# Kernel optimization log

Measured on AMD Instinct MI355X. Metric: run time of the kernel, lower is better.

Reference implementation:

```python
import jax, jax.numpy as jnp
import numpy as np

N, E = 8000, 128000
IN_DIM = OUT_DIM = REL_DIM = 64
NUM_RELS, NUM_BASES = 200, 50
R2 = 2 * NUM_RELS


def setup_inputs() -> dict:
    key = jax.random.key(0)
    ks = jax.random.split(key, 10)
    feat = jax.random.normal(ks[0], (N, IN_DIM), jnp.float32)
    rel_emb = jax.random.normal(ks[1], (R2, REL_DIM), jnp.float32)
    weight = jax.random.normal(ks[2], (NUM_BASES, IN_DIM, OUT_DIM), jnp.float32) * 0.05
    w_comp = jax.random.normal(ks[3], (R2, NUM_BASES), jnp.float32) * 0.1
    self_loop_weight = jax.random.normal(ks[4], (IN_DIM, OUT_DIM), jnp.float32) * 0.05
    W_R_w = jax.random.normal(ks[5], (REL_DIM, REL_DIM), jnp.float32) * 0.05
    W_R_b = jnp.zeros((REL_DIM,), jnp.float32)
    src = jax.random.randint(ks[6], (E,), 0, N, dtype=jnp.int32)
    dst = jax.random.randint(ks[7], (E,), 0, N, dtype=jnp.int32)
    etype = jax.random.randint(ks[8], (E,), 0, R2, dtype=jnp.int32)
    return dict(feat=feat, rel_emb=rel_emb, weight=weight, w_comp=w_comp,
                self_loop_weight=self_loop_weight, W_R_w=W_R_w, W_R_b=W_R_b,
                src=src, dst=dst, etype=etype)


def reference(feat, rel_emb, weight, w_comp, self_loop_weight, W_R_w, W_R_b,
              src, dst, etype):
    # rel_weight = (w_comp @ weight.view(B, in*out)).view(R2, in, out)
    rel_weight = jnp.einsum('rb,bio->rio', w_comp, weight)          # [R2, in, out]
    # msg_func: per-edge relation weight gather + bmm (gather-mm pattern)
    w_e = rel_weight[etype]                                          # [E, in, out]
    msg = jnp.einsum('ei,eio->eo', feat[src], w_e)                   # [E, out]
    # aggregator: alpha = 1/in_deg(dst) per edge -> weighted sum == mean over mailbox
    ones = jnp.ones((msg.shape[0],), msg.dtype)
    in_deg = jax.ops.segment_sum(ones, dst, num_segments=N)          # [N]
    nei_sum = jax.ops.segment_sum(msg, dst, num_segments=N)          # [N, out]
    nei_msg = nei_sum / jnp.maximum(in_deg, 1.0)[:, None]
    # curr_emb = dst_feat @ self_loop_weight (same for every edge into a node)
    curr_emb = feat @ self_loop_weight                               # [N, out]
    h = curr_emb + nei_msg                                           # no bias / no activation
    # is_input_layer=True: repr = cat([feat, h])
    repr_ = jnp.concatenate([feat, h], axis=1)                       # [N, in+out]
    # edge_update: W_R linear on relation embeddings (act is None)
    rel_emb_new = rel_emb @ W_R_w.T + W_R_b                          # [R2, rel_dim]
    return repr_, rel_emb_new
```

## Files before the change

### kernel.cpp

```cpp
#include <hip/hip_runtime.h>

#define N_NODES 8000
#define E_EDGES 128000
#define NUM_BASES 50
#define R2 400
#define CPR 4
#define RT 16

static __device__ __forceinline__ float bf2f(unsigned short u) {
    return __uint_as_float(((unsigned int)u) << 16);
}
static __device__ __forceinline__ unsigned short f2bf(float f) {
    unsigned int u = __float_as_uint(f);
    u += 0x7fffu + ((u >> 16) & 1u);
    return (unsigned short)(u >> 16);
}
static __device__ __forceinline__ float bcast(float v, int lane) {
    return __uint_as_float(__builtin_amdgcn_readlane(__float_as_uint(v), lane));
}

__global__ __launch_bounds__(256) void k_zero(int4* __restrict__ p, int n4) {
    const int i = blockIdx.x * 256 + threadIdx.x;
    if (i < n4) p[i] = make_int4(0, 0, 0, 0);
}

__global__ __launch_bounds__(256) void k_pre(const float* __restrict__ w_comp,
                                             const float* __restrict__ weight,
                                             unsigned short* __restrict__ relWh,
                                             const int* __restrict__ dst,
                                             const int* __restrict__ etype,
                                             int* __restrict__ cnt16,
                                             int* __restrict__ dcnt) {
    const int blk = blockIdx.x;
    const int t = threadIdx.x;
    if (blk < 100) {
        const int rt = blk >> 2;
        const int pb = blk & 3;
        const int r0 = rt * RT;
        const int p = pb * 256 + t;
        const float4* w4 = (const float4*)weight;
        float4 acc[RT];
#pragma unroll
        for (int rr = 0; rr < RT; ++rr) acc[rr] = make_float4(0.f, 0.f, 0.f, 0.f);
        for (int b = 0; b < NUM_BASES; ++b) {
            const float4 w = w4[b * 1024 + p];
#pragma unroll
            for (int rr = 0; rr < RT; ++rr) {
                const float c = w_comp[(r0 + rr) * NUM_BASES + b];
                acc[rr].x = fmaf(c, w.x, acc[rr].x);
                acc[rr].y = fmaf(c, w.y, acc[rr].y);
                acc[rr].z = fmaf(c, w.z, acc[rr].z);
                acc[rr].w = fmaf(c, w.w, acc[rr].w);
            }
        }
        ushort4* outh = (ushort4*)relWh;
#pragma unroll
        for (int rr = 0; rr < RT; ++rr) {
            ushort4 v;
            v.x = f2bf(acc[rr].x); v.y = f2bf(acc[rr].y);
            v.z = f2bf(acc[rr].z); v.w = f2bf(acc[rr].w);
            outh[(r0 + rr) * 1024 + p] = v;
        }
    } else {
        const int e = (blk - 100) * 256 + t;
        if (e >= E_EDGES) return;
        atomicAdd(&cnt16[etype[e] * 16], 1);
        atomicAdd(&dcnt[dst[e]], 1);
    }
}

__global__ __launch_bounds__(1024) void k_scan(const int* __restrict__ cnt16,
                                               const int* __restrict__ dcnt,
                                               int* __restrict__ off,
                                               int* __restrict__ doff,
                                               int* __restrict__ cursor16,
                                               int* __restrict__ dcursor) {
    __shared__ int s[1024];
    const int t = threadIdx.x;
    if (blockIdx.x == 0) {
        const int v = (t < R2) ? cnt16[t * 16] : 0;
        s[t] = v;
        __syncthreads();
        for (int d = 1; d < 1024; d <<= 1) {
            const int p = (t >= d) ? s[t - d] : 0;
            __syncthreads();
            s[t] += p;
            __syncthreads();
        }
        if (t == 0) off[0] = 0;
        if (t < R2) {
            off[t + 1] = s[t];
            cursor16[t * 16] = s[t] - v;
        }
    } else {
        const int base = t * 8;
        int loc[8];
        int run = 0;
#pragma unroll
        for (int q = 0; q < 8; ++q) {
            const int v = (base + q < N_NODES) ? dcnt[base + q] : 0;
            loc[q] = run;
            run += v;
        }
        s[t] = run;
        __syncthreads();
        for (int d = 1; d < 1024; d <<= 1) {
            const int p = (t >= d) ? s[t - d] : 0;
            __syncthreads();
            s[t] += p;
            __syncthreads();
        }
        const int ex = s[t] - run;
#pragma unroll
        for (int q = 0; q < 8; ++q) {
            if (base + q < N_NODES) {
                const int o = ex + loc[q];
                doff[base + q] = o;
                dcursor[base + q] = o;
            }
        }
        if (t == 1023) doff[N_NODES] = s[1023];
    }
}

__global__ __launch_bounds__(256) void k_scatter(const int* __restrict__ src,
                                                 const int* __restrict__ dst,
                                                 const int* __restrict__ etype,
                                                 int* __restrict__ cursor16,
                                                 int* __restrict__ dcursor,
                                                 int2* __restrict__ sedge,
                                                 int mode) {
    const int e = blockIdx.x * 256 + threadIdx.x;
    if (e >= E_EDGES) return;
    const int r = etype[e];
    const int d = dst[e];
    const int rpos = atomicAdd(&cursor16[r * 16], 1);
    int y;
    if (mode == 0) y = atomicAdd(&dcursor[d], 1);
    else           y = d;
    sedge[rpos] = make_int2(src[e], y);
}

__global__ __launch_bounds__(256) void k_edge(const float* __restrict__ feat,
                                              const unsigned short* __restrict__ relWh,
                                              const int2* __restrict__ sedge,
                                              const int* __restrict__ off,
                                              unsigned short* __restrict__ msg) {
    const int xcd = blockIdx.x & 7;
    const int j = blockIdx.x >> 3;
    const int r = xcd * 50 + (j >> 2);
    const int chunk = j & 3;
    const int lane = threadIdx.x & 63;
    const int wv = threadIdx.x >> 6;
    const int beg = off[r];
    const int cnt = off[r + 1] - beg;
    const int cbeg = beg + (cnt * chunk) / CPR;
    const int cend = beg + (cnt * (chunk + 1)) / CPR;

    const unsigned short* __restrict__ Wh = relWh + r * 4096;
    float w[64];
#pragma unroll
    for (int i = 0; i < 64; ++i) w[i] = bf2f(Wh[i * 64 + lane]);

    int idx = cbeg + wv;
    for (; idx + 4 < cend; idx += 8) {
        const int iB = idx + 4;
        const int2 eA = sedge[idx];
        const int2 eB = sedge[iB];
        const int sA = __builtin_amdgcn_readfirstlane(eA.x);
        const int dA = __builtin_amdgcn_readfirstlane(eA.y);
        const int sB = __builtin_amdgcn_readfirstlane(eB.x);
        const int dB = __builtin_amdgcn_readfirstlane(eB.y);
        const float* __restrict__ fA = feat + sA * 64;
        const float* __restrict__ fB = feat + sB * 64;
        float a0 = 0.f, a1 = 0.f, a2 = 0.f, a3 = 0.f;
        float b0 = 0.f, b1 = 0.f, b2 = 0.f, b3 = 0.f;
#pragma unroll
        for (int i = 0; i < 64; i += 4) {
            a0 = fmaf(fA[i    ], w[i    ], a0);  b0 = fmaf(fB[i    ], w[i    ], b0);
            a1 = fmaf(fA[i + 1], w[i + 1], a1);  b1 = fmaf(fB[i + 1], w[i + 1], b1);
            a2 = fmaf(fA[i + 2], w[i + 2], a2);  b2 = fmaf(fB[i + 2], w[i + 2], b2);
            a3 = fmaf(fA[i + 3], w[i + 3], a3);  b3 = fmaf(fB[i + 3], w[i + 3], b3);
        }
        msg[dA * 64 + lane] = f2bf((a0 + a1) + (a2 + a3));
        msg[dB * 64 + lane] = f2bf((b0 + b1) + (b2 + b3));
    }
    for (; idx < cend; idx += 4) {
        const int2 eA = sedge[idx];
        const int sA = __builtin_amdgcn_readfirstlane(eA.x);
        const int dA = __builtin_amdgcn_readfirstlane(eA.y);
        const float* __restrict__ frow = feat + sA * 64;
        float a0 = 0.f, a1 = 0.f, a2 = 0.f, a3 = 0.f;
#pragma unroll
        for (int i = 0; i < 64; i += 4) {
            a0 = fmaf(frow[i    ], w[i    ], a0);
            a1 = fmaf(frow[i + 1], w[i + 1], a1);
            a2 = fmaf(frow[i + 2], w[i + 2], a2);
            a3 = fmaf(frow[i + 3], w[i + 3], a3);
        }
        msg[dA * 64 + lane] = f2bf((a0 + a1) + (a2 + a3));
    }
}

__global__ __launch_bounds__(256) void k_edge_at(const float* __restrict__ feat,
                                                 const unsigned short* __restrict__ relWh,
                                                 const int2* __restrict__ sedge,
                                                 const int* __restrict__ off,
                                                 float* __restrict__ nei_sum) {
    const int xcd = blockIdx.x & 7;
    const int j = blockIdx.x >> 3;
    const int r = xcd * 50 + (j >> 2);
    const int chunk = j & 3;
    const int lane = threadIdx.x & 63;
    const int wv = threadIdx.x >> 6;
    const int beg = off[r];
    const int cnt = off[r + 1] - beg;
    const int cbeg = beg + (cnt * chunk) / CPR;
    const int cend = beg + (cnt * (chunk + 1)) / CPR;

    const unsigned short* __restrict__ Wh = relWh + r * 4096;
    float w[64];
#pragma unroll
    for (int i = 0; i < 64; ++i) w[i] = bf2f(Wh[i * 64 + lane]);

    for (int idx = cbeg + wv; idx < cend; idx += 4) {
        const int2 eA = sedge[idx];
        const int s = __builtin_amdgcn_readfirstlane(eA.x);
        const int d = __builtin_amdgcn_readfirstlane(eA.y);
        const float* __restrict__ frow = feat + s * 64;
        float a0 = 0.f, a1 = 0.f, a2 = 0.f, a3 = 0.f;
#pragma unroll
        for (int i = 0; i < 64; i += 4) {
            a0 = fmaf(frow[i    ], w[i    ], a0);
            a1 = fmaf(frow[i + 1], w[i + 1], a1);
            a2 = fmaf(frow[i + 2], w[i + 2], a2);
            a3 = fmaf(frow[i + 3], w[i + 3], a3);
        }
        atomicAdd(&nei_sum[d * 64 + lane], (a0 + a1) + (a2 + a3));
    }
}

__global__ __launch_bounds__(256) void k_post(const float* __restrict__ feat,
                                              const float* __restrict__ slw,
                                              const int* __restrict__ doff,
                                              const unsigned short* __restrict__ msg,
                                              const float* __restrict__ rel_emb,
                                              const float* __restrict__ Wr,
                                              const float* __restrict__ br,
                                              float* __restrict__ out) {
    __shared__ float s_w[4096];
    const int blk = blockIdx.x;
    const int t = threadIdx.x;
    const int lane = t & 63;
    const int wv = t >> 6;
    if (blk < 500) {
#pragma unroll
        for (int k = 0; k < 16; ++k) s_w[k * 256 + t] = slw[k * 256 + t];
        __syncthreads();
#pragma unroll
        for (int q = 0; q < 4; ++q) {
            const int n = blk * 16 + wv * 4 + q;
            const int b0 = doff[n];
            const int b1 = doff[n + 1];
            const float* __restrict__ frow = feat + n * 64;
            const float fa = frow[lane];
            float acc = 0.f;
#pragma unroll
            for (int i = 0; i < 64; ++i)
                acc = fmaf(frow[i], s_w[i * 64 + lane], acc);
            float sm = 0.f;
            int jj = b0;
            for (; jj + 1 < b1; jj += 2) {
                const float m0 = bf2f(msg[jj * 64 + lane]);
                const float m1 = bf2f(msg[(jj + 1) * 64 + lane]);
                sm += m0 + m1;
            }
            if (jj < b1) sm += bf2f(msg[jj * 64 + lane]);
            const float inv = 1.0f / fmaxf((float)(b1 - b0), 1.0f);
            out[n * 128 + lane] = fa;
            out[n * 128 + 64 + lane] = fmaf(sm, inv, acc);
        }
    } else {
#pragma unroll
        for (int k = 0; k < 16; ++k) {
            const int idx = k * 256 + t;
            s_w[(idx & 63) * 64 + (idx >> 6)] = Wr[idx];
        }
        __syncthreads();
        const int r = (blk - 500) * 4 + wv;
        const float re = rel_emb[r * 64 + lane];
        float acc = br[lane];
#pragma unroll
        for (int k = 0; k < 64; ++k)
            acc = fmaf(bcast(re, k), s_w[k * 64 + lane], acc);
        out[N_NODES * 128 + r * 64 + lane] = acc;
    }
}

__global__ __launch_bounds__(256) void k_post_at(const float* __restrict__ feat,
                                                 const float* __restrict__ slw,
                                                 const float* __restrict__ nei_sum,
                                                 const int* __restrict__ doff,
                                                 const float* __restrict__ rel_emb,
                                                 const float* __restrict__ Wr,
                                                 const float* __restrict__ br,
                                                 float* __restrict__ out) {
    __shared__ float s_w[4096];
    const int blk = blockIdx.x;
    const int t = threadIdx.x;
    const int lane = t & 63;
    const int wv = t >> 6;
    if (blk < 500) {
#pragma unroll
        for (int k = 0; k < 16; ++k) s_w[k * 256 + t] = slw[k * 256 + t];
        __syncthreads();
#pragma unroll
        for (int q = 0; q < 4; ++q) {
            const int n = blk * 16 + wv * 4 + q;
            const float* __restrict__ frow = feat + n * 64;
            const float fa = frow[lane];
            float acc = 0.f;
#pragma unroll
            for (int i = 0; i < 64; ++i)
                acc = fmaf(frow[i], s_w[i * 64 + lane], acc);
            const float deg = (float)(doff[n + 1] - doff[n]);
            const float inv = 1.0f / fmaxf(deg, 1.0f);
            out[n * 128 + lane] = fa;
            out[n * 128 + 64 + lane] = fmaf(nei_sum[n * 64 + lane], inv, acc);
        }
    } else {
#pragma unroll
        for (int k = 0; k < 16; ++k) {
            const int idx = k * 256 + t;
            s_w[(idx & 63) * 64 + (idx >> 6)] = Wr[idx];
        }
        __syncthreads();
        const int r = (blk - 500) * 4 + wv;
        const float re = rel_emb[r * 64 + lane];
        float acc = br[lane];
#pragma unroll
        for (int k = 0; k < 64; ++k)
            acc = fmaf(bcast(re, k), s_w[k * 64 + lane], acc);
        out[N_NODES * 128 + r * 64 + lane] = acc;
    }
}

extern "C" void kernel_launch(void* const* d_in, const int* in_sizes, int n_in,
                              void* d_out, int out_size, void* d_ws, size_t ws_size,
                              hipStream_t stream) {
    const float* feat    = (const float*)d_in[0];
    const float* rel_emb = (const float*)d_in[1];
    const float* weight  = (const float*)d_in[2];
    const float* w_comp  = (const float*)d_in[3];
    const float* slw     = (const float*)d_in[4];
    const float* Wr      = (const float*)d_in[5];
    const float* br      = (const float*)d_in[6];
    const int*   src     = (const int*)d_in[7];
    const int*   dst     = (const int*)d_in[8];
    const int*   etype   = (const int*)d_in[9];
    float* out = (float*)d_out;
    char* ws = (char*)d_ws;

    if (ws_size >= 20833728) {
        unsigned short* relWh = (unsigned short*)(ws);
        unsigned short* msg   = (unsigned short*)(ws + 3276800);
        int2* sedge   = (int2*)(ws + 19660800);
        int* off      = (int*)(ws + 20684800);
        int* doff     = (int*)(ws + 20686464);
        int* cnt16    = (int*)(ws + 20718528);
        int* dcnt     = (int*)(ws + 20744128);
        int* cursor16 = (int*)(ws + 20776128);
        int* dcursor  = (int*)(ws + 20801728);

        k_zero<<<15, 256, 0, stream>>>((int4*)cnt16, 3600);
        k_pre<<<600, 256, 0, stream>>>(w_comp, weight, relWh, dst, etype,
                                       cnt16, dcnt);
        k_scan<<<2, 1024, 0, stream>>>(cnt16, dcnt, off, doff, cursor16, dcursor);
        k_scatter<<<500, 256, 0, stream>>>(src, dst, etype, cursor16, dcursor,
                                           sedge, 0);
        k_edge<<<R2 * CPR, 256, 0, stream>>>(feat, relWh, sedge, off, msg);
        k_post<<<600, 256, 0, stream>>>(feat, slw, doff, msg, rel_emb, Wr, br,
                                        out);
    } else {
        unsigned short* relWh = (unsigned short*)(ws);
        int2* sedge   = (int2*)(ws + 3276800);
        int* off      = (int*)(ws + 4300800);
        int* doff     = (int*)(ws + 4302464);
        float* nei    = (float*)(ws + 4334528);
        int* cnt16    = (int*)(ws + 6382528);
        int* dcnt     = (int*)(ws + 6408128);
        int* cursor16 = (int*)(ws + 6440128);
        int* dcursor  = (int*)(ws + 6465728);

        k_zero<<<515, 256, 0, stream>>>((int4*)nei, 131600);
        k_pre<<<600, 256, 0, stream>>>(w_comp, weight, relWh, dst, etype,
                                       cnt16, dcnt);
        k_scan<<<2, 1024, 0, stream>>>(cnt16, dcnt, off, doff, cursor16, dcursor);
        k_scatter<<<500, 256, 0, stream>>>(src, dst, etype, cursor16, dcursor,
                                           sedge, 1);
        k_edge_at<<<R2 * CPR, 256, 0, stream>>>(feat, relWh, sedge, off, nei);
        k_post_at<<<600, 256, 0, stream>>>(feat, slw, nei, doff, rel_emb, Wr, br,
                                           out);
    }
}
```

Before: 119.1 us.

## Use per-block LDS histograms for edge bucketing and single-wave edge blocks

```diff
diff --git a/kernel.cpp b/kernel.cpp
--- a/kernel.cpp
+++ b/kernel.cpp
@@ -4,8 +4,10 @@
 #define E_EDGES 128000
 #define NUM_BASES 50
 #define R2 400
-#define CPR 4
+#define CPR 8
 #define RT 16
+#define HB 32
+#define EPB (E_EDGES / HB)
 
 static __device__ __forceinline__ float bf2f(unsigned short u) {
     return __uint_as_float(((unsigned int)u) << 16);
@@ -29,8 +31,8 @@
                                              unsigned short* __restrict__ relWh,
                                              const int* __restrict__ dst,
                                              const int* __restrict__ etype,
-                                             int* __restrict__ cnt16,
-                                             int* __restrict__ dcnt) {
+                                             int* __restrict__ bcnt,
+                                             int* __restrict__ dcnt16) {
     const int blk = blockIdx.x;
     const int t = threadIdx.x;
     if (blk < 100) {
@@ -62,96 +64,125 @@
             outh[(r0 + rr) * 1024 + p] = v;
         }
     } else {
-        const int e = (blk - 100) * 256 + t;
-        if (e >= E_EDGES) return;
-        atomicAdd(&cnt16[etype[e] * 16], 1);
-        atomicAdd(&dcnt[dst[e]], 1);
-    }
-}
-
-__global__ __launch_bounds__(1024) void k_scan(const int* __restrict__ cnt16,
-                                               const int* __restrict__ dcnt,
-                                               int* __restrict__ off,
-                                               int* __restrict__ doff,
-                                               int* __restrict__ cursor16,
-                                               int* __restrict__ dcursor) {
-    __shared__ int s[1024];
+        __shared__ int lcnt[R2];
+        const int hb = blk - 100;
+        for (int i = t; i < R2; i += 256) lcnt[i] = 0;
+        __syncthreads();
+        const int e0 = hb * EPB;
+        for (int e = e0 + t; e < e0 + EPB; e += 256) {
+            atomicAdd(&lcnt[etype[e]], 1);
+            atomicAdd(&dcnt16[dst[e] * 16], 1);
+        }
+        __syncthreads();
+        for (int i = t; i < R2; i += 256) bcnt[hb * R2 + i] = lcnt[i];
+    }
+}
+
+__global__ __launch_bounds__(512) void k_scan(const int* __restrict__ bcnt,
+                                              const int* __restrict__ dcnt16,
+                                              int* __restrict__ off,
+                                              int* __restrict__ doff,
+                                              int* __restrict__ bbase,
+                                              int* __restrict__ dcursor16) {
+    __shared__ int sh[8];
     const int t = threadIdx.x;
+    const int lane = t & 63;
+    const int wid = t >> 6;
     if (blockIdx.x == 0) {
-        const int v = (t < R2) ? cnt16[t * 16] : 0;
-        s[t] = v;
-        __syncthreads();
-        for (int d = 1; d < 1024; d <<= 1) {
-            const int p = (t >= d) ? s[t - d] : 0;
-            __syncthreads();
-            s[t] += p;
-            __syncthreads();
-        }
+        int tot = 0;
+        if (t < R2)
+            for (int b = 0; b < HB; ++b) tot += bcnt[b * R2 + t];
+        int v = tot;
+#pragma unroll
+        for (int d = 1; d < 64; d <<= 1) {
+            const int u = __shfl_up(v, d, 64);
+            if (lane >= d) v += u;
+        }
+        if (lane == 63) sh[wid] = v;
+        __syncthreads();
+        int wo = 0;
+        for (int i = 0; i < wid; ++i) wo += sh[i];
+        const int incl = v + wo;
+        const int ex = incl - tot;
         if (t == 0) off[0] = 0;
         if (t < R2) {
-            off[t + 1] = s[t];
-            cursor16[t * 16] = s[t] - v;
+            off[t + 1] = incl;
+            int run = ex;
+            for (int b = 0; b < HB; ++b) {
+                bbase[b * R2 + t] = run;
+                run += bcnt[b * R2 + t];
+            }
         }
     } else {
-        const int base = t * 8;
-        int loc[8];
+        int loc[32];
         int run = 0;
-#pragma unroll
-        for (int q = 0; q < 8; ++q) {
-            const int v = (base + q < N_NODES) ? dcnt[base + q] : 0;
-            loc[q] = run;
-            run += v;
-        }
-        s[t] = run;
-        __syncthreads();
-        for (int d = 1; d < 1024; d <<= 1) {
-            const int p = (t >= d) ? s[t - d] : 0;
-            __syncthreads();
-            s[t] += p;
-            __syncthreads();
-        }
-        const int ex = s[t] - run;
-#pragma unroll
-        for (int q = 0; q < 8; ++q) {
-            if (base + q < N_NODES) {
-                const int o = ex + loc[q];
-                doff[base + q] = o;
-                dcursor[base + q] = o;
-            }
-        }
-        if (t == 1023) doff[N_NODES] = s[1023];
+        const int base = t * 32;
+        if (t < 256) {
+#pragma unroll
+            for (int q = 0; q < 32; ++q) {
+                const int v = (base + q < N_NODES) ? dcnt16[(base + q) * 16] : 0;
+                loc[q] = run;
+                run += v;
+            }
+        }
+        int v = (t < 256) ? run : 0;
+#pragma unroll
+        for (int d = 1; d < 64; d <<= 1) {
+            const int u = __shfl_up(v, d, 64);
+            if (lane >= d) v += u;
+        }
+        if (lane == 63 && wid < 4) sh[wid] = v;
+        __syncthreads();
+        if (t < 256) {
+            int wo = 0;
+            for (int i = 0; i < wid; ++i) wo += sh[i];
+            const int incl = v + wo;
+            const int ex = incl - run;
+#pragma unroll
+            for (int q = 0; q < 32; ++q) {
+                if (base + q < N_NODES) {
+                    const int o = ex + loc[q];
+                    doff[base + q] = o;
+                    dcursor16[(base + q) * 16] = o;
+                }
+            }
+            if (t == 255) doff[N_NODES] = incl;
+        }
     }
 }
 
 __global__ __launch_bounds__(256) void k_scatter(const int* __restrict__ src,
                                                  const int* __restrict__ dst,
                                                  const int* __restrict__ etype,
-                                                 int* __restrict__ cursor16,
-                                                 int* __restrict__ dcursor,
-                                                 int2* __restrict__ sedge,
-                                                 int mode) {
-    const int e = blockIdx.x * 256 + threadIdx.x;
-    if (e >= E_EDGES) return;
-    const int r = etype[e];
-    const int d = dst[e];
-    const int rpos = atomicAdd(&cursor16[r * 16], 1);
-    int y;
-    if (mode == 0) y = atomicAdd(&dcursor[d], 1);
-    else           y = d;
-    sedge[rpos] = make_int2(src[e], y);
-}
-
-__global__ __launch_bounds__(256) void k_edge(const float* __restrict__ feat,
-                                              const unsigned short* __restrict__ relWh,
-                                              const int2* __restrict__ sedge,
-                                              const int* __restrict__ off,
-                                              unsigned short* __restrict__ msg) {
-    const int xcd = blockIdx.x & 7;
-    const int j = blockIdx.x >> 3;
-    const int r = xcd * 50 + (j >> 2);
-    const int chunk = j & 3;
-    const int lane = threadIdx.x & 63;
-    const int wv = threadIdx.x >> 6;
+                                                 const int* __restrict__ bbase,
+                                                 int* __restrict__ dcursor16,
+                                                 int2* __restrict__ sedge) {
+    __shared__ int lcur[R2];
+    const int blk = blockIdx.x;
+    const int t = threadIdx.x;
+    for (int i = t; i < R2; i += 256) lcur[i] = bbase[blk * R2 + i];
+    __syncthreads();
+    const int e0 = blk * EPB;
+    for (int e = e0 + t; e < e0 + EPB; e += 256) {
+        const int r = etype[e];
+        const int d = dst[e];
+        const int rpos = atomicAdd(&lcur[r], 1);
+        const int dpos = atomicAdd(&dcursor16[d * 16], 1);
+        sedge[rpos] = make_int2(src[e], dpos);
+    }
+}
+
+__global__ __launch_bounds__(64, 1) void k_edge(const float* __restrict__ feat,
+                                                const unsigned short* __restrict__ relWh,
+                                                const int2* __restrict__ sedge,
+                                                const int* __restrict__ off,
+                                                unsigned short* __restrict__ msg) {
+    const int blk = blockIdx.x;
+    const int xcd = blk & 7;
+    const int j = blk >> 3;
+    const int r = xcd * 50 + (j >> 3);
+    const int chunk = j & 7;
+    const int lane = threadIdx.x;
     const int beg = off[r];
     const int cnt = off[r + 1] - beg;
     const int cbeg = beg + (cnt * chunk) / CPR;
@@ -162,11 +193,10 @@
 #pragma unroll
     for (int i = 0; i < 64; ++i) w[i] = bf2f(Wh[i * 64 + lane]);
 
-    int idx = cbeg + wv;
-    for (; idx + 4 < cend; idx += 8) {
-        const int iB = idx + 4;
+    int idx = cbeg;
+    for (; idx + 1 < cend; idx += 2) {
         const int2 eA = sedge[idx];
-        const int2 eB = sedge[iB];
+        const int2 eB = sedge[idx + 1];
         const int sA = __builtin_amdgcn_readfirstlane(eA.x);
         const int dA = __builtin_amdgcn_readfirstlane(eA.y);
         const int sB = __builtin_amdgcn_readfirstlane(eB.x);
@@ -185,7 +215,7 @@
         msg[dA * 64 + lane] = f2bf((a0 + a1) + (a2 + a3));
         msg[dB * 64 + lane] = f2bf((b0 + b1) + (b2 + b3));
     }
-    for (; idx < cend; idx += 4) {
+    if (idx < cend) {
         const int2 eA = sedge[idx];
         const int sA = __builtin_amdgcn_readfirstlane(eA.x);
         const int dA = __builtin_amdgcn_readfirstlane(eA.y);
@@ -199,44 +229,6 @@
             a3 = fmaf(frow[i + 3], w[i + 3], a3);
         }
         msg[dA * 64 + lane] = f2bf((a0 + a1) + (a2 + a3));
-    }
-}
-
-__global__ __launch_bounds__(256) void k_edge_at(const float* __restrict__ feat,
-                                                 const unsigned short* __restrict__ relWh,
-                                                 const int2* __restrict__ sedge,
-                                                 const int* __restrict__ off,
-                                                 float* __restrict__ nei_sum) {
-    const int xcd = blockIdx.x & 7;
-    const int j = blockIdx.x >> 3;
-    const int r = xcd * 50 + (j >> 2);
-    const int chunk = j & 3;
-    const int lane = threadIdx.x & 63;
-    const int wv = threadIdx.x >> 6;
-    const int beg = off[r];
-    const int cnt = off[r + 1] - beg;
-    const int cbeg = beg + (cnt * chunk) / CPR;
-    const int cend = beg + (cnt * (chunk + 1)) / CPR;
-
-    const unsigned short* __restrict__ Wh = relWh + r * 4096;
-    float w[64];
-#pragma unroll
-    for (int i = 0; i < 64; ++i) w[i] = bf2f(Wh[i * 64 + lane]);
-
-    for (int idx = cbeg + wv; idx < cend; idx += 4) {
-        const int2 eA = sedge[idx];
-        const int s = __builtin_amdgcn_readfirstlane(eA.x);
-        const int d = __builtin_amdgcn_readfirstlane(eA.y);
-        const float* __restrict__ frow = feat + s * 64;
-        float a0 = 0.f, a1 = 0.f, a2 = 0.f, a3 = 0.f;
-#pragma unroll
-        for (int i = 0; i < 64; i += 4) {
-            a0 = fmaf(frow[i    ], w[i    ], a0);
-            a1 = fmaf(frow[i + 1], w[i + 1], a1);
-            a2 = fmaf(frow[i + 2], w[i + 2], a2);
-            a3 = fmaf(frow[i + 3], w[i + 3], a3);
-        }
-        atomicAdd(&nei_sum[d * 64 + lane], (a0 + a1) + (a2 + a3));
     }
 }
 
@@ -270,63 +262,17 @@
                 acc = fmaf(frow[i], s_w[i * 64 + lane], acc);
             float sm = 0.f;
             int jj = b0;
-            for (; jj + 1 < b1; jj += 2) {
+            for (; jj + 3 < b1; jj += 4) {
                 const float m0 = bf2f(msg[jj * 64 + lane]);
                 const float m1 = bf2f(msg[(jj + 1) * 64 + lane]);
-                sm += m0 + m1;
-            }
-            if (jj < b1) sm += bf2f(msg[jj * 64 + lane]);
+                const float m2 = bf2f(msg[(jj + 2) * 64 + lane]);
+                const float m3 = bf2f(msg[(jj + 3) * 64 + lane]);
+                sm += (m0 + m1) + (m2 + m3);
+            }
+            for (; jj < b1; ++jj) sm += bf2f(msg[jj * 64 + lane]);
             const float inv = 1.0f / fmaxf((float)(b1 - b0), 1.0f);
             out[n * 128 + lane] = fa;
             out[n * 128 + 64 + lane] = fmaf(sm, inv, acc);
-        }
-    } else {
-#pragma unroll
-        for (int k = 0; k < 16; ++k) {
-            const int idx = k * 256 + t;
-            s_w[(idx & 63) * 64 + (idx >> 6)] = Wr[idx];
-        }
-        __syncthreads();
-        const int r = (blk - 500) * 4 + wv;
-        const float re = rel_emb[r * 64 + lane];
-        float acc = br[lane];
-#pragma unroll
-        for (int k = 0; k < 64; ++k)
-            acc = fmaf(bcast(re, k), s_w[k * 64 + lane], acc);
-        out[N_NODES * 128 + r * 64 + lane] = acc;
-    }
-}
-
-__global__ __launch_bounds__(256) void k_post_at(const float* __restrict__ feat,
-                                                 const float* __restrict__ slw,
-                                                 const float* __restrict__ nei_sum,
-                                                 const int* __restrict__ doff,
-                                                 const float* __restrict__ rel_emb,
-                                                 const float* __restrict__ Wr,
-                                                 const float* __restrict__ br,
-                                                 float* __restrict__ out) {
-    __shared__ float s_w[4096];
-    const int blk = blockIdx.x;
-    const int t = threadIdx.x;
-    const int lane = t & 63;
-    const int wv = t >> 6;
-    if (blk < 500) {
-#pragma unroll
-        for (int k = 0; k < 16; ++k) s_w[k * 256 + t] = slw[k * 256 + t];
-        __syncthreads();
-#pragma unroll
-        for (int q = 0; q < 4; ++q) {
-            const int n = blk * 16 + wv * 4 + q;
-            const float* __restrict__ frow = feat + n * 64;
-            const float fa = frow[lane];
-            float acc = 0.f;
-#pragma unroll
-            for (int i = 0; i < 64; ++i)
-                acc = fmaf(frow[i], s_w[i * 64 + lane], acc);
-            const float deg = (float)(doff[n + 1] - doff[n]);
-            const float inv = 1.0f / fmaxf(deg, 1.0f);
-            out[n * 128 + lane] = fa;
-            out[n * 128 + 64 + lane] = fmaf(nei_sum[n * 64 + lane], inv, acc);
         }
     } else {
 #pragma unroll
@@ -361,45 +307,21 @@
     float* out = (float*)d_out;
     char* ws = (char*)d_ws;
 
-    if (ws_size >= 20833728) {
-        unsigned short* relWh = (unsigned short*)(ws);
-        unsigned short* msg   = (unsigned short*)(ws + 3276800);
-        int2* sedge   = (int2*)(ws + 19660800);
-        int* off      = (int*)(ws + 20684800);
-        int* doff     = (int*)(ws + 20686464);
-        int* cnt16    = (int*)(ws + 20718528);
-        int* dcnt     = (int*)(ws + 20744128);
-        int* cursor16 = (int*)(ws + 20776128);
-        int* dcursor  = (int*)(ws + 20801728);
-
-        k_zero<<<15, 256, 0, stream>>>((int4*)cnt16, 3600);
-        k_pre<<<600, 256, 0, stream>>>(w_comp, weight, relWh, dst, etype,
-                                       cnt16, dcnt);
-        k_scan<<<2, 1024, 0, stream>>>(cnt16, dcnt, off, doff, cursor16, dcursor);
-        k_scatter<<<500, 256, 0, stream>>>(src, dst, etype, cursor16, dcursor,
-                                           sedge, 0);
-        k_edge<<<R2 * CPR, 256, 0, stream>>>(feat, relWh, sedge, off, msg);
-        k_post<<<600, 256, 0, stream>>>(feat, slw, doff, msg, rel_emb, Wr, br,
-                                        out);
-    } else {
-        unsigned short* relWh = (unsigned short*)(ws);
-        int2* sedge   = (int2*)(ws + 3276800);
-        int* off      = (int*)(ws + 4300800);
-        int* doff     = (int*)(ws + 4302464);
-        float* nei    = (float*)(ws + 4334528);
-        int* cnt16    = (int*)(ws + 6382528);
-        int* dcnt     = (int*)(ws + 6408128);
-        int* cursor16 = (int*)(ws + 6440128);
-        int* dcursor  = (int*)(ws + 6465728);
-
-        k_zero<<<515, 256, 0, stream>>>((int4*)nei, 131600);
-        k_pre<<<600, 256, 0, stream>>>(w_comp, weight, relWh, dst, etype,
-                                       cnt16, dcnt);
-        k_scan<<<2, 1024, 0, stream>>>(cnt16, dcnt, off, doff, cursor16, dcursor);
-        k_scatter<<<500, 256, 0, stream>>>(src, dst, etype, cursor16, dcursor,
-                                           sedge, 1);
-        k_edge_at<<<R2 * CPR, 256, 0, stream>>>(feat, relWh, sedge, off, nei);
-        k_post_at<<<600, 256, 0, stream>>>(feat, slw, nei, doff, rel_emb, Wr, br,
-                                           out);
-    }
-}
+    unsigned short* relWh   = (unsigned short*)(ws);
+    unsigned short* msg     = (unsigned short*)(ws + 3276800);
+    int2* sedge     = (int2*)(ws + 19660800);
+    int* off        = (int*)(ws + 20684800);
+    int* doff       = (int*)(ws + 20686464);
+    int* bcnt       = (int*)(ws + 20718528);
+    int* bbase      = (int*)(ws + 20769728);
+    int* dcnt16     = (int*)(ws + 20820928);
+    int* dcursor16  = (int*)(ws + 21332928);
+
+    k_zero<<<125, 256, 0, stream>>>((int4*)dcnt16, 32000);
+    k_pre<<<132, 256, 0, stream>>>(w_comp, weight, relWh, dst, etype,
+                                   bcnt, dcnt16);
+    k_scan<<<2, 512, 0, stream>>>(bcnt, dcnt16, off, doff, bbase, dcursor16);
+    k_scatter<<<HB, 256, 0, stream>>>(src, dst, etype, bbase, dcursor16, sedge);
+    k_edge<<<R2 * CPR, 64, 0, stream>>>(feat, relWh, sedge, off, msg);
+    k_post<<<600, 256, 0, stream>>>(feat, slw, doff, msg, rel_emb, Wr, br, out);
+}
```

Result: no change. 117.1 us (-1.7%).
